# Optimization experiments

Measured on AMD Instinct MI355X. Metric: run time of the kernel, lower is better.

## Reference

```python
import jax, jax.numpy as jnp
import numpy as np

N, M, D, L = 8, 2048, 128, 128  # batch, num_nodes, input_dim, latent_dim


def setup_inputs() -> dict:
    key = jax.random.key(0)
    ks = jax.random.split(key, 9)
    s = 0.02
    return {
        "x": jax.random.normal(ks[0], (N, M, D), dtype=jnp.float32),
        # f_node: Linear(D, 2L) -> ReLU -> Linear(2L, L)
        "w1n": jax.random.normal(ks[1], (D, 2 * L), dtype=jnp.float32) * s,
        "b1n": jnp.zeros((2 * L,), dtype=jnp.float32),
        "w2n": jax.random.normal(ks[2], (2 * L, L), dtype=jnp.float32) * s,
        "b2n": jnp.zeros((L,), dtype=jnp.float32),
        # f_edge: Linear(2L, L) -> ReLU -> Linear(L, 1)
        "w1e": jax.random.normal(ks[3], (2 * L, L), dtype=jnp.float32) * s,
        "b1e": jnp.zeros((L,), dtype=jnp.float32),
        "w2e": jax.random.normal(ks[4], (L, 1), dtype=jnp.float32) * s,
        "b2e": jnp.zeros((1,), dtype=jnp.float32),
    }


def reference(x, w1n, b1n, w2n, b2n, w1e, b1e, w2e, b2e):
    n, m, _ = x.shape
    # f_node MLP: (N, m, D) -> (N, m, L)
    h = jnp.maximum(x @ w1n + b1n, 0.0) @ w2n + b2n
    # In the original, the double transpose on `receiver` cancels, so the
    # edge feature is concat(x_i, x_i) for every (i, j) pair: independent of j.
    # Compute per-node then broadcast across j (identical math, no O(m^2 * 2L) blowup).
    pair = jnp.concatenate([h, h], axis=-1)              # (N, m, 2L)
    e = jnp.maximum(pair @ w1e + b1e, 0.0) @ w2e + b2e   # (N, m, 1)
    e = e / m
    edge = jnp.broadcast_to(e, (n, m, m))                # edge[b, i, j] = e[b, i]
    return h, edge
```

## Files before the change

### kernel.cpp

```cpp
#include <hip/hip_runtime.h>


typedef short short8 __attribute__((ext_vector_type(8)));
typedef float floatx4 __attribute__((ext_vector_type(4)));

__device__ __forceinline__ short f2bf(float f) {
    union { float f; unsigned u; } v; v.f = f;
    unsigned r = v.u + 0x7fffu + ((v.u >> 16) & 1u);
    return (short)(r >> 16);
}

__global__ __launch_bounds__(256)
void prep_weights(const float* __restrict__ w1n, const float* __restrict__ w2n,
                  const float* __restrict__ w1e, short* __restrict__ ws)
{
    const int id = blockIdx.x * 256 + threadIdx.x;
    const int j = id & 7;
    if (id < 32768) {
        const int g = id >> 3, l = g & 63, ctk = g >> 6;
        const int ct = ctk >> 2, k = ctk & 3;
        const int kg = k * 32 + (l >> 4) * 8 + j;
        ws[id] = f2bf(w1n[kg * 256 + ct * 16 + (l & 15)]);
    } else if (id < 65536) {
        const int g = (id - 32768) >> 3, l = g & 63, ctk = g >> 6;
        const int ct = ctk >> 3, k = ctk & 7;
        const int kg = k * 32 + (l >> 4) * 8 + j;
        ws[id] = f2bf(w2n[kg * 128 + ct * 16 + (l & 15)]);
    } else {
        const int g = (id - 65536) >> 3, l = g & 63, ctk = g >> 6;
        const int ct = ctk >> 2, k = ctk & 3;
        const int kg = k * 32 + (l >> 4) * 8 + j;
        ws[id] = f2bf(w1e[kg * 128 + ct * 16 + (l & 15)]
                      + w1e[(kg + 128) * 128 + ct * 16 + (l & 15)]);
    }
}

#define TPB 256
#define ROWS 16
#define NTILES 1024
#define GRID 512
#define XS_STRIDE 136
#define H1_STRIDE 264

__global__ __launch_bounds__(TPB, 2)
void fused_persistent(const float* __restrict__ x,
                      const float* __restrict__ b1n, const float* __restrict__ b2n,
                      const float* __restrict__ b1e,
                      const float* __restrict__ w2e, const float* __restrict__ b2e,
                      const short* __restrict__ wt,
                      float* __restrict__ h_out, float* __restrict__ edge_out)
{
    __shared__ short xs[ROWS * XS_STRIDE];
    __shared__ short h1s[ROWS * H1_STRIDE];
    __shared__ short hbs[ROWS * XS_STRIDE];
    __shared__ float partial[4][ROWS];
    __shared__ float es[ROWS];

    const int t = threadIdx.x;
    const int w = t >> 6;
    const int l = t & 63;
    const int l15 = l & 15;
    const int quad = l >> 4;

    const short* __restrict__ W2S = wt + 32768;
    const short* __restrict__ WES = wt + 65536;

    for (int vb = blockIdx.x; vb < NTILES; vb += GRID) {
        const int row0 = vb * ROWS;

        {
            const float4* __restrict__ x4 = (const float4*)(x + (size_t)row0 * 128);
#pragma unroll
            for (int i = 0; i < 2; ++i) {
                const int fi = t + i * TPB;
                const float4 v = x4[fi];
                const int row = fi >> 5, col = (fi & 31) * 4;
                short4 s;
                s.x = f2bf(v.x); s.y = f2bf(v.y); s.z = f2bf(v.z); s.w = f2bf(v.w);
                *(short4*)&xs[row * XS_STRIDE + col] = s;
            }
        }
        __syncthreads();

        {
            short8 a1[4];
#pragma unroll
            for (int k = 0; k < 4; ++k)
                a1[k] = *(const short8*)&xs[l15 * XS_STRIDE + k * 32 + quad * 8];

            floatx4 acc1[4];
#pragma unroll
            for (int ci = 0; ci < 4; ++ci) {
                const int ct = 4 * w + ci;
                const float b = b1n[ct * 16 + l15];
                acc1[ci] = (floatx4){b, b, b, b};
#pragma unroll
                for (int k = 0; k < 4; ++k) {
                    const short8 bf = *(const short8*)(wt + ((ct * 4 + k) * 64 + l) * 8);
                    acc1[ci] = __builtin_amdgcn_mfma_f32_16x16x32_bf16(a1[k], bf, acc1[ci], 0, 0, 0);
                }
            }
#pragma unroll
            for (int ci = 0; ci < 4; ++ci) {
                const int ct = 4 * w + ci;
#pragma unroll
                for (int r = 0; r < 4; ++r)
                    h1s[(quad * 4 + r) * H1_STRIDE + ct * 16 + l15] = f2bf(fmaxf(acc1[ci][r], 0.f));
            }
        }
        __syncthreads();

        {
            short8 a2[8];
#pragma unroll
            for (int k = 0; k < 8; ++k)
                a2[k] = *(const short8*)&h1s[l15 * H1_STRIDE + k * 32 + quad * 8];

#pragma unroll
            for (int ci = 0; ci < 2; ++ci) {
                const int ct = 2 * w + ci;
                const float b = b2n[ct * 16 + l15];
                floatx4 acc2 = (floatx4){b, b, b, b};
#pragma unroll
                for (int k = 0; k < 8; ++k) {
                    const short8 bf = *(const short8*)(W2S + ((ct * 8 + k) * 64 + l) * 8);
                    acc2 = __builtin_amdgcn_mfma_f32_16x16x32_bf16(a2[k], bf, acc2, 0, 0, 0);
                }
#pragma unroll
                for (int r = 0; r < 4; ++r) {
                    const int row = quad * 4 + r;
                    const float v = acc2[r];
                    h_out[(size_t)(row0 + row) * 128 + ct * 16 + l15] = v;
                    hbs[row * XS_STRIDE + ct * 16 + l15] = f2bf(v);
                }
            }
        }
        __syncthreads();

        {
            short8 a3[4];
#pragma unroll
            for (int k = 0; k < 4; ++k)
                a3[k] = *(const short8*)&hbs[l15 * XS_STRIDE + k * 32 + quad * 8];

            float p[4] = {0.f, 0.f, 0.f, 0.f};
#pragma unroll
            for (int ci = 0; ci < 2; ++ci) {
                const int ct = 2 * w + ci;
                const float b = b1e[ct * 16 + l15];
                floatx4 acc3 = (floatx4){b, b, b, b};
#pragma unroll
                for (int k = 0; k < 4; ++k) {
                    const short8 bf = *(const short8*)(WES + ((ct * 4 + k) * 64 + l) * 8);
                    acc3 = __builtin_amdgcn_mfma_f32_16x16x32_bf16(a3[k], bf, acc3, 0, 0, 0);
                }
                const float wv = w2e[ct * 16 + l15];
#pragma unroll
                for (int r = 0; r < 4; ++r)
                    p[r] += fmaxf(acc3[r], 0.f) * wv;
            }
#pragma unroll
            for (int off = 8; off >= 1; off >>= 1)
#pragma unroll
                for (int r = 0; r < 4; ++r)
                    p[r] += __shfl_xor(p[r], off, 64);
            if (l15 == 0) {
#pragma unroll
                for (int r = 0; r < 4; ++r)
                    partial[w][quad * 4 + r] = p[r];
            }
        }
        __syncthreads();
        if (t < ROWS) {
            es[t] = (partial[0][t] + partial[1][t] + partial[2][t]
                     + partial[3][t] + b2e[0]) * (1.0f / 2048.0f);
        }
        __syncthreads();

        {
            floatx4* __restrict__ e4 = (floatx4*)(edge_out + (size_t)row0 * 2048);
#pragma unroll
            for (int r = 0; r < ROWS; ++r) {
                const float ev = es[r];
                const floatx4 vv = (floatx4){ev, ev, ev, ev};
                e4[r * 512 + t] = vv;
                e4[r * 512 + t + 256] = vv;
            }
        }
    }
}

extern "C" void kernel_launch(void* const* d_in, const int* in_sizes, int n_in,
                              void* d_out, int out_size, void* d_ws, size_t ws_size,
                              hipStream_t stream) {
    const float* x   = (const float*)d_in[0];
    const float* w1n = (const float*)d_in[1];
    const float* b1n = (const float*)d_in[2];
    const float* w2n = (const float*)d_in[3];
    const float* b2n = (const float*)d_in[4];
    const float* w1e = (const float*)d_in[5];
    const float* b1e = (const float*)d_in[6];
    const float* w2e = (const float*)d_in[7];
    const float* b2e = (const float*)d_in[8];

    float* h_out    = (float*)d_out;
    float* edge_out = (float*)d_out + (size_t)8 * 2048 * 128;
    short* wt       = (short*)d_ws;

    prep_weights<<<dim3(320), dim3(256), 0, stream>>>(w1n, w2n, w1e, wt);
    fused_persistent<<<dim3(GRID), dim3(TPB), 0, stream>>>(
        x, b1n, b2n, b1e, w2e, b2e, wt, h_out, edge_out);
}
```

Measured before the change: 164.6 us.

## Give each wave its own 16-row tile and drop block-level barriers

Replaces the persistent 512-block kernel, where four waves split the column tiles of a shared 16-row tile, with a 256-block grid in which each wave processes its own 16-row tile end to end. x is read straight from global memory into MFMA operand registers, and each wave keeps private LDS buffers, so all __syncthreads and the cross-wave partial reduction go away. Each wave now streams the full weight set on its own, which multiplies weight traffic through L1/L2. Launch bounds drop to one block per CU, and the grid of 1024 waves may leave some CUs underused.

```diff
diff --git a/kernel.cpp b/kernel.cpp
--- a/kernel.cpp
+++ b/kernel.cpp
@@ -36,156 +36,124 @@
 }
 
 #define TPB 256
-#define ROWS 16
-#define NTILES 1024
-#define GRID 512
-#define XS_STRIDE 136
 #define H1_STRIDE 264
+#define HB_STRIDE 136
 
-__global__ __launch_bounds__(TPB, 2)
-void fused_persistent(const float* __restrict__ x,
-                      const float* __restrict__ b1n, const float* __restrict__ b2n,
-                      const float* __restrict__ b1e,
-                      const float* __restrict__ w2e, const float* __restrict__ b2e,
-                      const short* __restrict__ wt,
-                      float* __restrict__ h_out, float* __restrict__ edge_out)
+__global__ __launch_bounds__(TPB, 1)
+void fused_wavetile(const float* __restrict__ x,
+                    const float* __restrict__ b1n, const float* __restrict__ b2n,
+                    const float* __restrict__ b1e,
+                    const float* __restrict__ w2e, const float* __restrict__ b2e,
+                    const short* __restrict__ wt,
+                    float* __restrict__ h_out, float* __restrict__ edge_out)
 {
-    __shared__ short xs[ROWS * XS_STRIDE];
-    __shared__ short h1s[ROWS * H1_STRIDE];
-    __shared__ short hbs[ROWS * XS_STRIDE];
-    __shared__ float partial[4][ROWS];
-    __shared__ float es[ROWS];
+    __shared__ short h1s_all[4 * 16 * H1_STRIDE];
+    __shared__ short hbs_all[4 * 16 * HB_STRIDE];
+    __shared__ float es_all[4 * 16];
 
     const int t = threadIdx.x;
-    const int w = t >> 6;
+    const int wave = t >> 6;
     const int l = t & 63;
     const int l15 = l & 15;
     const int quad = l >> 4;
+    const int row0 = (blockIdx.x * 4 + wave) * 16;
+
+    short* __restrict__ h1w = h1s_all + wave * 16 * H1_STRIDE;
+    short* __restrict__ hbw = hbs_all + wave * 16 * HB_STRIDE;
+    float* __restrict__ esw = es_all + wave * 16;
 
     const short* __restrict__ W2S = wt + 32768;
     const short* __restrict__ WES = wt + 65536;
 
-    for (int vb = blockIdx.x; vb < NTILES; vb += GRID) {
-        const int row0 = vb * ROWS;
-
-        {
-            const float4* __restrict__ x4 = (const float4*)(x + (size_t)row0 * 128);
+    short8 a1[4];
 #pragma unroll
-            for (int i = 0; i < 2; ++i) {
-                const int fi = t + i * TPB;
-                const float4 v = x4[fi];
-                const int row = fi >> 5, col = (fi & 31) * 4;
-                short4 s;
-                s.x = f2bf(v.x); s.y = f2bf(v.y); s.z = f2bf(v.z); s.w = f2bf(v.w);
-                *(short4*)&xs[row * XS_STRIDE + col] = s;
-            }
-        }
-        __syncthreads();
-
-        {
-            short8 a1[4];
-#pragma unroll
-            for (int k = 0; k < 4; ++k)
-                a1[k] = *(const short8*)&xs[l15 * XS_STRIDE + k * 32 + quad * 8];
-
-            floatx4 acc1[4];
-#pragma unroll
-            for (int ci = 0; ci < 4; ++ci) {
-                const int ct = 4 * w + ci;
-                const float b = b1n[ct * 16 + l15];
-                acc1[ci] = (floatx4){b, b, b, b};
-#pragma unroll
-                for (int k = 0; k < 4; ++k) {
-                    const short8 bf = *(const short8*)(wt + ((ct * 4 + k) * 64 + l) * 8);
-                    acc1[ci] = __builtin_amdgcn_mfma_f32_16x16x32_bf16(a1[k], bf, acc1[ci], 0, 0, 0);
-                }
-            }
-#pragma unroll
-            for (int ci = 0; ci < 4; ++ci) {
-                const int ct = 4 * w + ci;
-#pragma unroll
-                for (int r = 0; r < 4; ++r)
-                    h1s[(quad * 4 + r) * H1_STRIDE + ct * 16 + l15] = f2bf(fmaxf(acc1[ci][r], 0.f));
-            }
-        }
-        __syncthreads();
-
-        {
-            short8 a2[8];
-#pragma unroll
-            for (int k = 0; k < 8; ++k)
-                a2[k] = *(const short8*)&h1s[l15 * H1_STRIDE + k * 32 + quad * 8];
+    for (int k = 0; k < 4; ++k) {
+        const float* p = x + (size_t)(row0 + l15) * 128 + k * 32 + quad * 8;
+        const float4 v0 = *(const float4*)p;
+        const float4 v1 = *(const float4*)(p + 4);
+        short8 a;
+        a[0] = f2bf(v0.x); a[1] = f2bf(v0.y); a[2] = f2bf(v0.z); a[3] = f2bf(v0.w);
+        a[4] = f2bf(v1.x); a[5] = f2bf(v1.y); a[6] = f2bf(v1.z); a[7] = f2bf(v1.w);
+        a1[k] = a;
+    }
 
 #pragma unroll
-            for (int ci = 0; ci < 2; ++ci) {
-                const int ct = 2 * w + ci;
-                const float b = b2n[ct * 16 + l15];
-                floatx4 acc2 = (floatx4){b, b, b, b};
+    for (int ct = 0; ct < 16; ++ct) {
+        const float b = b1n[ct * 16 + l15];
+        floatx4 acc = (floatx4){b, b, b, b};
 #pragma unroll
-                for (int k = 0; k < 8; ++k) {
-                    const short8 bf = *(const short8*)(W2S + ((ct * 8 + k) * 64 + l) * 8);
-                    acc2 = __builtin_amdgcn_mfma_f32_16x16x32_bf16(a2[k], bf, acc2, 0, 0, 0);
-                }
+        for (int k = 0; k < 4; ++k) {
+            const short8 bf = *(const short8*)(wt + ((ct * 4 + k) * 64 + l) * 8);
+            acc = __builtin_amdgcn_mfma_f32_16x16x32_bf16(a1[k], bf, acc, 0, 0, 0);
+        }
 #pragma unroll
-                for (int r = 0; r < 4; ++r) {
-                    const int row = quad * 4 + r;
-                    const float v = acc2[r];
-                    h_out[(size_t)(row0 + row) * 128 + ct * 16 + l15] = v;
-                    hbs[row * XS_STRIDE + ct * 16 + l15] = f2bf(v);
-                }
-            }
+        for (int r = 0; r < 4; ++r)
+            h1w[(quad * 4 + r) * H1_STRIDE + ct * 16 + l15] = f2bf(fmaxf(acc[r], 0.f));
+    }
+
+    short8 a2[8];
+#pragma unroll
+    for (int k = 0; k < 8; ++k)
+        a2[k] = *(const short8*)&h1w[l15 * H1_STRIDE + k * 32 + quad * 8];
+
+#pragma unroll
+    for (int ct = 0; ct < 8; ++ct) {
+        const float b = b2n[ct * 16 + l15];
+        floatx4 acc = (floatx4){b, b, b, b};
+#pragma unroll
+        for (int k = 0; k < 8; ++k) {
+            const short8 bf = *(const short8*)(W2S + ((ct * 8 + k) * 64 + l) * 8);
+            acc = __builtin_amdgcn_mfma_f32_16x16x32_bf16(a2[k], bf, acc, 0, 0, 0);
         }
-        __syncthreads();
+#pragma unroll
+        for (int r = 0; r < 4; ++r) {
+            const int row = quad * 4 + r;
+            h_out[(size_t)(row0 + row) * 128 + ct * 16 + l15] = acc[r];
+            hbw[row * HB_STRIDE + ct * 16 + l15] = f2bf(acc[r]);
+        }
+    }
 
-        {
-            short8 a3[4];
+    short8 a3[4];
 #pragma unroll
-            for (int k = 0; k < 4; ++k)
-                a3[k] = *(const short8*)&hbs[l15 * XS_STRIDE + k * 32 + quad * 8];
+    for (int k = 0; k < 4; ++k)
+        a3[k] = *(const short8*)&hbw[l15 * HB_STRIDE + k * 32 + quad * 8];
 
-            float p[4] = {0.f, 0.f, 0.f, 0.f};
+    float p[4] = {0.f, 0.f, 0.f, 0.f};
 #pragma unroll
-            for (int ci = 0; ci < 2; ++ci) {
-                const int ct = 2 * w + ci;
-                const float b = b1e[ct * 16 + l15];
-                floatx4 acc3 = (floatx4){b, b, b, b};
+    for (int ct = 0; ct < 8; ++ct) {
+        const float b = b1e[ct * 16 + l15];
+        floatx4 acc = (floatx4){b, b, b, b};
 #pragma unroll
-                for (int k = 0; k < 4; ++k) {
-                    const short8 bf = *(const short8*)(WES + ((ct * 4 + k) * 64 + l) * 8);
-                    acc3 = __builtin_amdgcn_mfma_f32_16x16x32_bf16(a3[k], bf, acc3, 0, 0, 0);
-                }
-                const float wv = w2e[ct * 16 + l15];
+        for (int k = 0; k < 4; ++k) {
+            const short8 bf = *(const short8*)(WES + ((ct * 4 + k) * 64 + l) * 8);
+            acc = __builtin_amdgcn_mfma_f32_16x16x32_bf16(a3[k], bf, acc, 0, 0, 0);
+        }
+        const float wv = w2e[ct * 16 + l15];
 #pragma unroll
-                for (int r = 0; r < 4; ++r)
-                    p[r] += fmaxf(acc3[r], 0.f) * wv;
-            }
+        for (int r = 0; r < 4; ++r)
+            p[r] += fmaxf(acc[r], 0.f) * wv;
+    }
 #pragma unroll
-            for (int off = 8; off >= 1; off >>= 1)
+    for (int off = 8; off >= 1; off >>= 1)
 #pragma unroll
-                for (int r = 0; r < 4; ++r)
-                    p[r] += __shfl_xor(p[r], off, 64);
-            if (l15 == 0) {
+        for (int r = 0; r < 4; ++r)
+            p[r] += __shfl_xor(p[r], off, 64);
+    if (l15 == 0) {
+        const float bb = b2e[0];
 #pragma unroll
-                for (int r = 0; r < 4; ++r)
-                    partial[w][quad * 4 + r] = p[r];
-            }
-        }
-        __syncthreads();
-        if (t < ROWS) {
-            es[t] = (partial[0][t] + partial[1][t] + partial[2][t]
-                     + partial[3][t] + b2e[0]) * (1.0f / 2048.0f);
-        }
-        __syncthreads();
+        for (int r = 0; r < 4; ++r)
+            esw[quad * 4 + r] = (p[r] + bb) * (1.0f / 2048.0f);
+    }
 
-        {
-            floatx4* __restrict__ e4 = (floatx4*)(edge_out + (size_t)row0 * 2048);
+    {
+        floatx4* __restrict__ e4 = (floatx4*)(edge_out + (size_t)row0 * 2048);
 #pragma unroll
-            for (int r = 0; r < ROWS; ++r) {
-                const float ev = es[r];
-                const floatx4 vv = (floatx4){ev, ev, ev, ev};
-                e4[r * 512 + t] = vv;
-                e4[r * 512 + t + 256] = vv;
-            }
+        for (int r = 0; r < 16; ++r) {
+            const float ev = esw[r];
+            const floatx4 vv = (floatx4){ev, ev, ev, ev};
+#pragma unroll
+            for (int i = 0; i < 8; ++i)
+                e4[r * 512 + i * 64 + l] = vv;
         }
     }
 }
@@ -208,6 +176,6 @@
     short* wt       = (short*)d_ws;
 
     prep_weights<<<dim3(320), dim3(256), 0, stream>>>(w1n, w2n, w1e, wt);
-    fused_persistent<<<dim3(GRID), dim3(TPB), 0, stream>>>(
+    fused_wavetile<<<dim3(256), dim3(TPB), 0, stream>>>(
         x, b1n, b2n, b1e, w2e, b2e, wt, h_out, edge_out);
 }
```

After: 201.1 us. +22.2%, slower.
